# Kernel tuning notes

Measured on AMD Instinct MI355X. Metric: run time of the kernel, lower is better.

## Reference

```python
import jax, jax.numpy as jnp
import numpy as np

NEG_INF = -1e18  # fp32 masking constant used by the original module


def setup_inputs() -> dict:
    key0 = jax.random.key(0)
    kq, kk, kv, km, ke = jax.random.split(key0, 5)
    B, L, H, C = 2, 2048, 16, 64
    query = jax.random.normal(kq, (B, L, H, C), dtype=jnp.float32)
    key = jax.random.normal(kk, (B, L, H, C), dtype=jnp.float32)
    value = jax.random.normal(kv, (B, L, H, C), dtype=jnp.float32)
    mask = jax.random.randint(km, (B, L, L), 0, 2).astype(jnp.bool_)
    edge_scores = jax.random.normal(ke, (1, H, L, L), dtype=jnp.float32)
    return {"query": query, "key": key, "value": value, "mask": mask,
            "edge_scores": edge_scores}


def _masked_softmax(att_score, mask):
    # mask: True -> keep, False -> masked. Fill with -1e18 (fp32 path),
    # softmax, then multiply by mask (post-softmax zeroing), as in original.
    s = jnp.where(mask, att_score, NEG_INF)
    w = jax.nn.softmax(s, axis=-1)
    return w * mask.astype(w.dtype)


def reference(query, key, value, mask, edge_scores):
    # layout 'NTK': query/key/value (B, L, H, C); mask (B, Lq, Lm)
    scale = jnp.sqrt(jnp.asarray(query.shape[-1], dtype=query.dtype))
    # scores: (B, H, Lq, Lm)
    scores = jnp.einsum('binc,bjnc->bnij', query, key)
    scores = scores + edge_scores
    attn_weights = _masked_softmax(scores / scale, mask[:, None, :, :])
    # dropout rate is 0.0 -> identity
    # context: (B, Lq, H, Cv) -> (B, Lq, H*Cv)
    context = jnp.einsum('bnij,bjnc->binc', attn_weights, value)
    B, Lq = context.shape[0], context.shape[1]
    context_vec = context.reshape(B, Lq, -1)
    return (context_vec, scores, attn_weights)
```

## Files before the change

### kernel.cpp

```cpp
#include <hip/hip_runtime.h>
#include <hip/hip_bf16.h>


typedef __attribute__((ext_vector_type(8))) short bf16x8;
typedef __attribute__((ext_vector_type(4))) float f32x4;

#define LQ 2048
#define NH 16
#define CD 64

__device__ inline short f2bf(float x) {
    union { float f; unsigned u; } v; v.f = x;
    unsigned r = v.u + 0x7FFFu + ((v.u >> 16) & 1u);
    return (short)(r >> 16);
}

__device__ inline float wave_max(float v) {
    #pragma unroll
    for (int o = 32; o > 0; o >>= 1) v = fmaxf(v, __shfl_xor(v, o, 64));
    return v;
}
__device__ inline float wave_sum(float v) {
    #pragma unroll
    for (int o = 32; o > 0; o >>= 1) v += __shfl_xor(v, o, 64);
    return v;
}

__global__ __launch_bounds__(256)
void k_scores(const float* __restrict__ q, const float* __restrict__ kk,
              const float* __restrict__ edge, float* __restrict__ sc)
{
    __shared__ short Qs[64][72];
    __shared__ short Ks[64][72];
    const int z = blockIdx.z;
    const int b = z & 1, h = z >> 1;
    const int i0 = blockIdx.y * 64, j0 = blockIdx.x * 64;
    const int tid = threadIdx.x;
    const int r = tid >> 2, seg = (tid & 3) * 16;

    const float* qrow = q  + ((size_t)((b * LQ + i0 + r) * NH + h)) * CD + seg;
    const float* krow = kk + ((size_t)((b * LQ + j0 + r) * NH + h)) * CD + seg;
    #pragma unroll
    for (int u = 0; u < 4; ++u) {
        float4 f = ((const float4*)qrow)[u];
        *(short4*)&Qs[r][seg + u * 4] = make_short4(f2bf(f.x), f2bf(f.y), f2bf(f.z), f2bf(f.w));
        float4 g = ((const float4*)krow)[u];
        *(short4*)&Ks[r][seg + u * 4] = make_short4(f2bf(g.x), f2bf(g.y), f2bf(g.z), f2bf(g.w));
    }
    __syncthreads();

    const int wave = tid >> 6, lane = tid & 63;
    const int quad = lane >> 4, mm = lane & 15;

    bf16x8 a0 = *(const bf16x8*)&Qs[wave * 16 + mm][quad * 8];
    bf16x8 a1 = *(const bf16x8*)&Qs[wave * 16 + mm][32 + quad * 8];

    f32x4 acc[4];
    #pragma unroll
    for (int jt = 0; jt < 4; ++jt) {
        bf16x8 b0 = *(const bf16x8*)&Ks[jt * 16 + mm][quad * 8];
        bf16x8 b1 = *(const bf16x8*)&Ks[jt * 16 + mm][32 + quad * 8];
        f32x4 a = {0.f, 0.f, 0.f, 0.f};
        a = __builtin_amdgcn_mfma_f32_16x16x32_bf16(a0, b0, a, 0, 0, 0);
        a = __builtin_amdgcn_mfma_f32_16x16x32_bf16(a1, b1, a, 0, 0, 0);
        acc[jt] = a;
    }

    const int irow = i0 + wave * 16 + quad * 4;
    #pragma unroll
    for (int jt = 0; jt < 4; ++jt) {
        const int j = j0 + jt * 16 + mm;
        #pragma unroll
        for (int reg = 0; reg < 4; ++reg) {
            const int i = irow + reg;
            const size_t eidx = ((size_t)(h * LQ + i)) * LQ + j;
            const size_t sidx = ((size_t)((b * NH + h) * LQ + i)) * LQ + j;
            sc[sidx] = acc[jt][reg] + edge[eidx];
        }
    }
}

__global__ __launch_bounds__(256)
void k_softmax(const float* __restrict__ sc, const int* __restrict__ mask,
               float* __restrict__ attn)
{
    const int wave = threadIdx.x >> 6, lane = threadIdx.x & 63;
    const int gw = blockIdx.x * 4 + wave;
    const int bh = gw >> 11;
    const int i  = gw & 2047;
    const int b  = bh >> 4;

    const float* srow = sc + (size_t)gw * LQ;
    const int*   mrow = mask + ((size_t)(b * LQ + i)) * LQ;

    float sv[32];
    float vmax = -3.0e38f;
    #pragma unroll
    for (int t = 0; t < 8; ++t) {
        const int j = t * 256 + lane * 4;
        float4 s = *(const float4*)(srow + j);
        int4   m = *(const int4*)(mrow + j);
        sv[t * 4 + 0] = m.x ? s.x * 0.125f : -1.0e18f;
        sv[t * 4 + 1] = m.y ? s.y * 0.125f : -1.0e18f;
        sv[t * 4 + 2] = m.z ? s.z * 0.125f : -1.0e18f;
        sv[t * 4 + 3] = m.w ? s.w * 0.125f : -1.0e18f;
        vmax = fmaxf(vmax, fmaxf(fmaxf(sv[t*4], sv[t*4+1]), fmaxf(sv[t*4+2], sv[t*4+3])));
    }
    vmax = wave_max(vmax);

    float psum = 0.f;
    #pragma unroll
    for (int t = 0; t < 32; ++t) {
        sv[t] = __expf(sv[t] - vmax);
        psum += sv[t];
    }
    psum = wave_sum(psum);
    const float inv = (vmax < -9.0e17f) ? 0.f : 1.f / psum;

    float* arow = attn + (size_t)gw * LQ;
    #pragma unroll
    for (int t = 0; t < 8; ++t) {
        float4 o;
        o.x = sv[t*4+0] * inv; o.y = sv[t*4+1] * inv;
        o.z = sv[t*4+2] * inv; o.w = sv[t*4+3] * inv;
        *(float4*)(arow + t * 256 + lane * 4) = o;
    }
}

__global__ __launch_bounds__(256)
void k_pv(const float* __restrict__ attn, const float* __restrict__ v,
          float* __restrict__ out0)
{
    __shared__ short Ws[64][72];
    __shared__ short Vt[64][72];
    const int y = blockIdx.y;
    const int b = y & 1, h = y >> 1;
    const int i0 = blockIdx.x * 64;
    const int tid = threadIdx.x;
    const int r = tid >> 2, seg = (tid & 3) * 16;
    const int wave = tid >> 6, lane = tid & 63;
    const int quad = lane >> 4, mm = lane & 15;
    const int bh = b * NH + h;

    f32x4 acc[4] = { {0,0,0,0}, {0,0,0,0}, {0,0,0,0}, {0,0,0,0} };

    for (int kb = 0; kb < 32; ++kb) {
        const int j0 = kb * 64;
        const float* wrow = attn + ((size_t)(bh * LQ + i0 + r)) * LQ + j0 + seg;
        const float* vrow = v + ((size_t)((b * LQ + j0 + r) * NH + h)) * CD + seg;
        #pragma unroll
        for (int u = 0; u < 4; ++u) {
            float4 f = ((const float4*)wrow)[u];
            *(short4*)&Ws[r][seg + u * 4] = make_short4(f2bf(f.x), f2bf(f.y), f2bf(f.z), f2bf(f.w));
            float4 g = ((const float4*)vrow)[u];
            Vt[seg + u * 4 + 0][r] = f2bf(g.x);
            Vt[seg + u * 4 + 1][r] = f2bf(g.y);
            Vt[seg + u * 4 + 2][r] = f2bf(g.z);
            Vt[seg + u * 4 + 3][r] = f2bf(g.w);
        }
        __syncthreads();

        #pragma unroll
        for (int kt = 0; kt < 2; ++kt) {
            bf16x8 a = *(const bf16x8*)&Ws[wave * 16 + mm][kt * 32 + quad * 8];
            #pragma unroll
            for (int nt = 0; nt < 4; ++nt) {
                bf16x8 bb = *(const bf16x8*)&Vt[nt * 16 + mm][kt * 32 + quad * 8];
                acc[nt] = __builtin_amdgcn_mfma_f32_16x16x32_bf16(a, bb, acc[nt], 0, 0, 0);
            }
        }
        __syncthreads();
    }

    const int irow = i0 + wave * 16 + quad * 4;
    #pragma unroll
    for (int nt = 0; nt < 4; ++nt) {
        const int c = nt * 16 + mm;
        #pragma unroll
        for (int reg = 0; reg < 4; ++reg) {
            const int i = irow + reg;
            out0[((size_t)(b * LQ + i)) * (NH * CD) + h * CD + c] = acc[nt][reg];
        }
    }
}

extern "C" void kernel_launch(void* const* d_in, const int* in_sizes, int n_in,
                              void* d_out, int out_size, void* d_ws, size_t ws_size,
                              hipStream_t stream) {
    const float* q    = (const float*)d_in[0];
    const float* k    = (const float*)d_in[1];
    const float* v    = (const float*)d_in[2];
    const int*   mask = (const int*)d_in[3];
    const float* edge = (const float*)d_in[4];

    float* out = (float*)d_out;
    float* ctx = out;
    float* sc  = out + 4194304;
    float* at  = sc + 134217728;

    k_scores <<<dim3(32, 32, 32), 256, 0, stream>>>(q, k, edge, sc);
    k_softmax<<<dim3(16384), 256, 0, stream>>>(sc, mask, at);
    k_pv     <<<dim3(32, 32), 256, 0, stream>>>(at, v, ctx);
}
```

Baseline: 1.723 ms.

## Fuse scores, softmax and PV into two-pass flash-style kernels

Replaces the three kernels (scores, softmax, PV) with two. The first pass recomputes QK^T per row block and keeps an online max and sum-exp for each row in a small workspace. The second pass recomputes the scores, writes the scores and normalized weights, and feeds the bf16 weights straight into the PV MFMA through LDS. This removes the full read-back of the 512MB score and attention matrices by the softmax and PV kernels. In exchange, QK^T is computed twice, edge and mask are read twice, and each block now loops sequentially over all key blocks with narrow scalar global accesses.

```diff
diff --git a/kernel.cpp b/kernel.cpp
--- a/kernel.cpp
+++ b/kernel.cpp
@@ -15,37 +15,24 @@
     return (short)(r >> 16);
 }
 
-__device__ inline float wave_max(float v) {
-    #pragma unroll
-    for (int o = 32; o > 0; o >>= 1) v = fmaxf(v, __shfl_xor(v, o, 64));
-    return v;
-}
-__device__ inline float wave_sum(float v) {
-    #pragma unroll
-    for (int o = 32; o > 0; o >>= 1) v += __shfl_xor(v, o, 64);
-    return v;
-}
-
 __global__ __launch_bounds__(256)
-void k_scores(const float* __restrict__ q, const float* __restrict__ kk,
-              const float* __restrict__ edge, float* __restrict__ sc)
+void k_stats(const float* __restrict__ q, const float* __restrict__ kk,
+             const float* __restrict__ edge, const int* __restrict__ mask,
+             float2* __restrict__ stats)
 {
     __shared__ short Qs[64][72];
     __shared__ short Ks[64][72];
-    const int z = blockIdx.z;
+    const int z = blockIdx.y;
     const int b = z & 1, h = z >> 1;
-    const int i0 = blockIdx.y * 64, j0 = blockIdx.x * 64;
+    const int i0 = blockIdx.x * 64;
     const int tid = threadIdx.x;
     const int r = tid >> 2, seg = (tid & 3) * 16;
 
-    const float* qrow = q  + ((size_t)((b * LQ + i0 + r) * NH + h)) * CD + seg;
-    const float* krow = kk + ((size_t)((b * LQ + j0 + r) * NH + h)) * CD + seg;
+    const float* qrow = q + ((size_t)((b * LQ + i0 + r) * NH + h)) * CD + seg;
     #pragma unroll
     for (int u = 0; u < 4; ++u) {
         float4 f = ((const float4*)qrow)[u];
         *(short4*)&Qs[r][seg + u * 4] = make_short4(f2bf(f.x), f2bf(f.y), f2bf(f.z), f2bf(f.w));
-        float4 g = ((const float4*)krow)[u];
-        *(short4*)&Ks[r][seg + u * 4] = make_short4(f2bf(g.x), f2bf(g.y), f2bf(g.z), f2bf(g.w));
     }
     __syncthreads();
 
@@ -55,131 +42,175 @@
     bf16x8 a0 = *(const bf16x8*)&Qs[wave * 16 + mm][quad * 8];
     bf16x8 a1 = *(const bf16x8*)&Qs[wave * 16 + mm][32 + quad * 8];
 
-    f32x4 acc[4];
-    #pragma unroll
-    for (int jt = 0; jt < 4; ++jt) {
-        bf16x8 b0 = *(const bf16x8*)&Ks[jt * 16 + mm][quad * 8];
-        bf16x8 b1 = *(const bf16x8*)&Ks[jt * 16 + mm][32 + quad * 8];
-        f32x4 a = {0.f, 0.f, 0.f, 0.f};
-        a = __builtin_amdgcn_mfma_f32_16x16x32_bf16(a0, b0, a, 0, 0, 0);
-        a = __builtin_amdgcn_mfma_f32_16x16x32_bf16(a1, b1, a, 0, 0, 0);
-        acc[jt] = a;
-    }
-
     const int irow = i0 + wave * 16 + quad * 4;
-    #pragma unroll
-    for (int jt = 0; jt < 4; ++jt) {
-        const int j = j0 + jt * 16 + mm;
+    float m[4] = {-3.0e38f, -3.0e38f, -3.0e38f, -3.0e38f};
+    float l[4] = {0.f, 0.f, 0.f, 0.f};
+
+    for (int jb = 0; jb < 32; ++jb) {
+        const int j0 = jb * 64;
+        __syncthreads();
+        const float* krow = kk + ((size_t)((b * LQ + j0 + r) * NH + h)) * CD + seg;
+        #pragma unroll
+        for (int u = 0; u < 4; ++u) {
+            float4 g = ((const float4*)krow)[u];
+            *(short4*)&Ks[r][seg + u * 4] = make_short4(f2bf(g.x), f2bf(g.y), f2bf(g.z), f2bf(g.w));
+        }
+        __syncthreads();
+
+        f32x4 acc[4];
+        #pragma unroll
+        for (int jt = 0; jt < 4; ++jt) {
+            bf16x8 b0 = *(const bf16x8*)&Ks[jt * 16 + mm][quad * 8];
+            bf16x8 b1 = *(const bf16x8*)&Ks[jt * 16 + mm][32 + quad * 8];
+            f32x4 a = {0.f, 0.f, 0.f, 0.f};
+            a = __builtin_amdgcn_mfma_f32_16x16x32_bf16(a0, b0, a, 0, 0, 0);
+            a = __builtin_amdgcn_mfma_f32_16x16x32_bf16(a1, b1, a, 0, 0, 0);
+            acc[jt] = a;
+        }
+
+        float mv[4][4];
+        #pragma unroll
+        for (int jt = 0; jt < 4; ++jt) {
+            const int j = j0 + jt * 16 + mm;
+            #pragma unroll
+            for (int reg = 0; reg < 4; ++reg) {
+                const int i = irow + reg;
+                const float e = edge[((size_t)(h * LQ + i)) * LQ + j];
+                const int   mk = mask[((size_t)(b * LQ + i)) * LQ + j];
+                const float x = acc[jt][reg] + e;
+                mv[jt][reg] = mk ? x * 0.125f : -1.0e18f;
+            }
+        }
         #pragma unroll
         for (int reg = 0; reg < 4; ++reg) {
-            const int i = irow + reg;
-            const size_t eidx = ((size_t)(h * LQ + i)) * LQ + j;
-            const size_t sidx = ((size_t)((b * NH + h) * LQ + i)) * LQ + j;
-            sc[sidx] = acc[jt][reg] + edge[eidx];
+            float tm = fmaxf(fmaxf(mv[0][reg], mv[1][reg]), fmaxf(mv[2][reg], mv[3][reg]));
+            #pragma unroll
+            for (int o = 1; o <= 8; o <<= 1) tm = fmaxf(tm, __shfl_xor(tm, o, 64));
+            const float m2 = fmaxf(m[reg], tm);
+            float ps = __expf(mv[0][reg] - m2) + __expf(mv[1][reg] - m2)
+                     + __expf(mv[2][reg] - m2) + __expf(mv[3][reg] - m2);
+            #pragma unroll
+            for (int o = 1; o <= 8; o <<= 1) ps += __shfl_xor(ps, o, 64);
+            l[reg] = l[reg] * __expf(m[reg] - m2) + ps;
+            m[reg] = m2;
+        }
+    }
+
+    if (mm == 0) {
+        #pragma unroll
+        for (int reg = 0; reg < 4; ++reg) {
+            const size_t rid = (size_t)(b * NH + h) * LQ + irow + reg;
+            stats[rid] = make_float2(m[reg], l[reg]);
         }
     }
 }
 
 __global__ __launch_bounds__(256)
-void k_softmax(const float* __restrict__ sc, const int* __restrict__ mask,
-               float* __restrict__ attn)
+void k_fused(const float* __restrict__ q, const float* __restrict__ kk,
+             const float* __restrict__ v, const int* __restrict__ mask,
+             const float* __restrict__ edge, const float2* __restrict__ stats,
+             float* __restrict__ sc, float* __restrict__ attn,
+             float* __restrict__ ctx)
 {
-    const int wave = threadIdx.x >> 6, lane = threadIdx.x & 63;
-    const int gw = blockIdx.x * 4 + wave;
-    const int bh = gw >> 11;
-    const int i  = gw & 2047;
-    const int b  = bh >> 4;
-
-    const float* srow = sc + (size_t)gw * LQ;
-    const int*   mrow = mask + ((size_t)(b * LQ + i)) * LQ;
-
-    float sv[32];
-    float vmax = -3.0e38f;
-    #pragma unroll
-    for (int t = 0; t < 8; ++t) {
-        const int j = t * 256 + lane * 4;
-        float4 s = *(const float4*)(srow + j);
-        int4   m = *(const int4*)(mrow + j);
-        sv[t * 4 + 0] = m.x ? s.x * 0.125f : -1.0e18f;
-        sv[t * 4 + 1] = m.y ? s.y * 0.125f : -1.0e18f;
-        sv[t * 4 + 2] = m.z ? s.z * 0.125f : -1.0e18f;
-        sv[t * 4 + 3] = m.w ? s.w * 0.125f : -1.0e18f;
-        vmax = fmaxf(vmax, fmaxf(fmaxf(sv[t*4], sv[t*4+1]), fmaxf(sv[t*4+2], sv[t*4+3])));
-    }
-    vmax = wave_max(vmax);
-
-    float psum = 0.f;
-    #pragma unroll
-    for (int t = 0; t < 32; ++t) {
-        sv[t] = __expf(sv[t] - vmax);
-        psum += sv[t];
-    }
-    psum = wave_sum(psum);
-    const float inv = (vmax < -9.0e17f) ? 0.f : 1.f / psum;
-
-    float* arow = attn + (size_t)gw * LQ;
-    #pragma unroll
-    for (int t = 0; t < 8; ++t) {
-        float4 o;
-        o.x = sv[t*4+0] * inv; o.y = sv[t*4+1] * inv;
-        o.z = sv[t*4+2] * inv; o.w = sv[t*4+3] * inv;
-        *(float4*)(arow + t * 256 + lane * 4) = o;
-    }
-}
-
-__global__ __launch_bounds__(256)
-void k_pv(const float* __restrict__ attn, const float* __restrict__ v,
-          float* __restrict__ out0)
-{
-    __shared__ short Ws[64][72];
+    __shared__ short Qs[64][72];
+    __shared__ short Ks[64][72];
     __shared__ short Vt[64][72];
-    const int y = blockIdx.y;
-    const int b = y & 1, h = y >> 1;
+    __shared__ short Wt[4][16][72];
+
+    const int z = blockIdx.y;
+    const int b = z & 1, h = z >> 1;
     const int i0 = blockIdx.x * 64;
     const int tid = threadIdx.x;
     const int r = tid >> 2, seg = (tid & 3) * 16;
+
+    const float* qrow = q + ((size_t)((b * LQ + i0 + r) * NH + h)) * CD + seg;
+    #pragma unroll
+    for (int u = 0; u < 4; ++u) {
+        float4 f = ((const float4*)qrow)[u];
+        *(short4*)&Qs[r][seg + u * 4] = make_short4(f2bf(f.x), f2bf(f.y), f2bf(f.z), f2bf(f.w));
+    }
+    __syncthreads();
+
     const int wave = tid >> 6, lane = tid & 63;
     const int quad = lane >> 4, mm = lane & 15;
-    const int bh = b * NH + h;
-
-    f32x4 acc[4] = { {0,0,0,0}, {0,0,0,0}, {0,0,0,0}, {0,0,0,0} };
-
-    for (int kb = 0; kb < 32; ++kb) {
-        const int j0 = kb * 64;
-        const float* wrow = attn + ((size_t)(bh * LQ + i0 + r)) * LQ + j0 + seg;
-        const float* vrow = v + ((size_t)((b * LQ + j0 + r) * NH + h)) * CD + seg;
+
+    bf16x8 a0 = *(const bf16x8*)&Qs[wave * 16 + mm][quad * 8];
+    bf16x8 a1 = *(const bf16x8*)&Qs[wave * 16 + mm][32 + quad * 8];
+
+    const int irow = i0 + wave * 16 + quad * 4;
+    float msv[4], inv[4];
+    #pragma unroll
+    for (int reg = 0; reg < 4; ++reg) {
+        float2 st = stats[(size_t)(b * NH + h) * LQ + irow + reg];
+        msv[reg] = st.x;
+        inv[reg] = (st.x < -9.0e17f) ? 0.f : 1.f / st.y;
+    }
+
+    f32x4 cacc[4] = { {0,0,0,0}, {0,0,0,0}, {0,0,0,0}, {0,0,0,0} };
+
+    for (int jb = 0; jb < 32; ++jb) {
+        const int j0 = jb * 64;
+        __syncthreads();
+        const float* krow = kk + ((size_t)((b * LQ + j0 + r) * NH + h)) * CD + seg;
+        const float* vrow = v  + ((size_t)((b * LQ + j0 + r) * NH + h)) * CD + seg;
         #pragma unroll
         for (int u = 0; u < 4; ++u) {
-            float4 f = ((const float4*)wrow)[u];
-            *(short4*)&Ws[r][seg + u * 4] = make_short4(f2bf(f.x), f2bf(f.y), f2bf(f.z), f2bf(f.w));
-            float4 g = ((const float4*)vrow)[u];
-            Vt[seg + u * 4 + 0][r] = f2bf(g.x);
-            Vt[seg + u * 4 + 1][r] = f2bf(g.y);
-            Vt[seg + u * 4 + 2][r] = f2bf(g.z);
-            Vt[seg + u * 4 + 3][r] = f2bf(g.w);
-        }
-        __syncthreads();
+            float4 g = ((const float4*)krow)[u];
+            *(short4*)&Ks[r][seg + u * 4] = make_short4(f2bf(g.x), f2bf(g.y), f2bf(g.z), f2bf(g.w));
+            float4 w = ((const float4*)vrow)[u];
+            Vt[seg + u * 4 + 0][r] = f2bf(w.x);
+            Vt[seg + u * 4 + 1][r] = f2bf(w.y);
+            Vt[seg + u * 4 + 2][r] = f2bf(w.z);
+            Vt[seg + u * 4 + 3][r] = f2bf(w.w);
+        }
+        __syncthreads();
+
+        f32x4 acc[4];
+        #pragma unroll
+        for (int jt = 0; jt < 4; ++jt) {
+            bf16x8 b0 = *(const bf16x8*)&Ks[jt * 16 + mm][quad * 8];
+            bf16x8 b1 = *(const bf16x8*)&Ks[jt * 16 + mm][32 + quad * 8];
+            f32x4 a = {0.f, 0.f, 0.f, 0.f};
+            a = __builtin_amdgcn_mfma_f32_16x16x32_bf16(a0, b0, a, 0, 0, 0);
+            a = __builtin_amdgcn_mfma_f32_16x16x32_bf16(a1, b1, a, 0, 0, 0);
+            acc[jt] = a;
+        }
+
+        #pragma unroll
+        for (int jt = 0; jt < 4; ++jt) {
+            const int j = j0 + jt * 16 + mm;
+            #pragma unroll
+            for (int reg = 0; reg < 4; ++reg) {
+                const int i = irow + reg;
+                const size_t eidx = ((size_t)(h * LQ + i)) * LQ + j;
+                const size_t sidx = ((size_t)((b * NH + h) * LQ + i)) * LQ + j;
+                const float s = acc[jt][reg] + edge[eidx];
+                sc[sidx] = s;
+                const int mk = mask[((size_t)(b * LQ + i)) * LQ + j];
+                const float w = mk ? __expf(s * 0.125f - msv[reg]) * inv[reg] : 0.f;
+                attn[sidx] = w;
+                Wt[wave][quad * 4 + reg][jt * 16 + mm] = f2bf(w);
+            }
+        }
 
         #pragma unroll
         for (int kt = 0; kt < 2; ++kt) {
-            bf16x8 a = *(const bf16x8*)&Ws[wave * 16 + mm][kt * 32 + quad * 8];
+            bf16x8 aw = *(const bf16x8*)&Wt[wave][mm][kt * 32 + quad * 8];
             #pragma unroll
             for (int nt = 0; nt < 4; ++nt) {
                 bf16x8 bb = *(const bf16x8*)&Vt[nt * 16 + mm][kt * 32 + quad * 8];
-                acc[nt] = __builtin_amdgcn_mfma_f32_16x16x32_bf16(a, bb, acc[nt], 0, 0, 0);
+                cacc[nt] = __builtin_amdgcn_mfma_f32_16x16x32_bf16(aw, bb, cacc[nt], 0, 0, 0);
             }
         }
-        __syncthreads();
-    }
-
-    const int irow = i0 + wave * 16 + quad * 4;
+    }
+
     #pragma unroll
     for (int nt = 0; nt < 4; ++nt) {
         const int c = nt * 16 + mm;
         #pragma unroll
         for (int reg = 0; reg < 4; ++reg) {
             const int i = irow + reg;
-            out0[((size_t)(b * LQ + i)) * (NH * CD) + h * CD + c] = acc[nt][reg];
+            ctx[((size_t)(b * LQ + i)) * (NH * CD) + h * CD + c] = cacc[nt][reg];
         }
     }
 }
@@ -198,7 +229,8 @@
     float* sc  = out + 4194304;
     float* at  = sc + 134217728;
 
-    k_scores <<<dim3(32, 32, 32), 256, 0, stream>>>(q, k, edge, sc);
-    k_softmax<<<dim3(16384), 256, 0, stream>>>(sc, mask, at);
-    k_pv     <<<dim3(32, 32), 256, 0, stream>>>(at, v, ctx);
-}
+    float2* stats = (float2*)d_ws;
+
+    k_stats<<<dim3(32, 32), 256, 0, stream>>>(q, k, edge, mask, stats);
+    k_fused<<<dim3(32, 32), 256, 0, stream>>>(q, k, v, mask, edge, stats, sc, at, ctx);
+}
```

After: 2.030 ms. 1.18x slower.
